# Performance work log

Measured on AMD Instinct MI355X. Metric: run time of the kernel, lower is better.

## Reference

```python
import jax, jax.numpy as jnp
import numpy as np

B, F, K = 8192, 4096, 64


def setup_inputs() -> dict:
    key = jax.random.key(0)
    kx, kv = jax.random.split(key)
    x = jax.random.normal(kx, (B, F), dtype=jnp.float32)
    # original init: uniform(-0.01, 0.01)
    v = jax.random.uniform(kv, (F, K), dtype=jnp.float32, minval=-0.01, maxval=0.01)
    return {"x": x, "v": v}


def reference(x, v):
    # sum_{i<j} <v_i, v_j> x_i x_j  ==  0.5 * sum_f ((x@v)_f^2 - (x^2 @ v^2)_f)
    xv = x @ v                      # [B, K]
    x2v2 = (x * x) @ (v * v)        # [B, K]
    res = 0.5 * jnp.sum(xv * xv - x2v2, axis=-1, keepdims=True)  # [B, 1]
    return res
```

## Files before the change

### kernel.cpp

```cpp
#include <hip/hip_runtime.h>
#include <hip/hip_bf16.h>


#define F_DIM 4096
#define K_DIM 64
#define B_ROWS 8192

typedef __attribute__((ext_vector_type(8))) short short8;
typedef __attribute__((ext_vector_type(4))) float float4v;

__device__ __forceinline__ short f2bs(float f) {
    __hip_bfloat16 h = __float2bfloat16(f);
    short s;
    __builtin_memcpy(&s, &h, 2);
    return s;
}

__global__ void prep_kernel(const float* __restrict__ v,
                            __hip_bfloat16* __restrict__ vt,
                            float* __restrict__ w) {
    const int wave = (blockIdx.x * blockDim.x + threadIdx.x) >> 6;
    const int lane = threadIdx.x & 63;
    if (wave >= F_DIM) return;
    const float val = v[wave * K_DIM + lane];
    float sq = val * val;
#pragma unroll
    for (int m = 32; m >= 1; m >>= 1) sq += __shfl_xor(sq, m, 64);
    if (lane == 0) w[wave] = sq;
    vt[(size_t)lane * F_DIM + wave] = __float2bfloat16(val);
}

__launch_bounds__(512, 4)
__global__ void fm_main_kernel(const float* __restrict__ x,
                               const __hip_bfloat16* __restrict__ vt,
                               const float* __restrict__ w,
                               float* __restrict__ out) {
    __shared__ float yred[8][16][64];
    __shared__ float s2s[16];
    __shared__ float s1s[16];

    const int tid  = threadIdx.x;
    const int lane = tid & 63;
    const int wid  = tid >> 6;
    const int lrow = lane & 15;
    const int lk8  = (lane >> 4) * 8;
    const int row0 = blockIdx.x * 16;

    if (tid < 16) s2s[tid] = 0.0f;
    __syncthreads();

    const float* xrow = x + (size_t)(row0 + lrow) * F_DIM;

    float4v acc0 = {0.f,0.f,0.f,0.f}, acc1 = {0.f,0.f,0.f,0.f};
    float4v acc2 = {0.f,0.f,0.f,0.f}, acc3 = {0.f,0.f,0.f,0.f};
    float s2p = 0.0f;

    const int fbase = wid * (F_DIM / 8);

#pragma unroll 4
    for (int ks = 0; ks < (F_DIM / 8) / 32; ++ks) {
        const int fo = fbase + ks * 32 + lk8;
        const float4v xa = *(const float4v*)(xrow + fo);
        const float4v xb = *(const float4v*)(xrow + fo + 4);
        const float4v wa = *(const float4v*)(w + fo);
        const float4v wb = *(const float4v*)(w + fo + 4);

        s2p += xa.x*xa.x*wa.x + xa.y*xa.y*wa.y + xa.z*xa.z*wa.z + xa.w*xa.w*wa.w
             + xb.x*xb.x*wb.x + xb.y*xb.y*wb.y + xb.z*xb.z*wb.z + xb.w*xb.w*wb.w;

        short8 af;
        af[0]=f2bs(xa.x); af[1]=f2bs(xa.y); af[2]=f2bs(xa.z); af[3]=f2bs(xa.w);
        af[4]=f2bs(xb.x); af[5]=f2bs(xb.y); af[6]=f2bs(xb.z); af[7]=f2bs(xb.w);

        const __hip_bfloat16* bbase = vt + (size_t)lrow * F_DIM + fo;
        const short8 b0 = *(const short8*)(bbase);
        const short8 b1 = *(const short8*)(bbase + 16 * F_DIM);
        const short8 b2 = *(const short8*)(bbase + 32 * F_DIM);
        const short8 b3 = *(const short8*)(bbase + 48 * F_DIM);

        acc0 = __builtin_amdgcn_mfma_f32_16x16x32_bf16(af, b0, acc0, 0, 0, 0);
        acc1 = __builtin_amdgcn_mfma_f32_16x16x32_bf16(af, b1, acc1, 0, 0, 0);
        acc2 = __builtin_amdgcn_mfma_f32_16x16x32_bf16(af, b2, acc2, 0, 0, 0);
        acc3 = __builtin_amdgcn_mfma_f32_16x16x32_bf16(af, b3, acc3, 0, 0, 0);
    }

    s2p += __shfl_xor(s2p, 16, 64);
    s2p += __shfl_xor(s2p, 32, 64);
    if (lane < 16) atomicAdd(&s2s[lrow], s2p);

    const int arow = (lane >> 4) * 4;
#pragma unroll
    for (int r = 0; r < 4; ++r) {
        yred[wid][arow + r][ 0 + lrow] = acc0[r];
        yred[wid][arow + r][16 + lrow] = acc1[r];
        yred[wid][arow + r][32 + lrow] = acc2[r];
        yred[wid][arow + r][48 + lrow] = acc3[r];
    }
    __syncthreads();

#pragma unroll
    for (int half = 0; half < 2; ++half) {
        const int row = wid + half * 8;
        float y = 0.0f;
#pragma unroll
        for (int wv = 0; wv < 8; ++wv) y += yred[wv][row][lane];
        float yy = y * y;
#pragma unroll
        for (int m = 32; m >= 1; m >>= 1) yy += __shfl_xor(yy, m, 64);
        if (lane == 0) s1s[row] = yy;
    }
    __syncthreads();

    if (tid < 16) out[row0 + tid] = 0.5f * (s1s[tid] - s2s[tid]);
}

extern "C" void kernel_launch(void* const* d_in, const int* in_sizes, int n_in,
                              void* d_out, int out_size, void* d_ws, size_t ws_size,
                              hipStream_t stream) {
    const float* x = (const float*)d_in[0];
    const float* v = (const float*)d_in[1];
    float* out = (float*)d_out;

    __hip_bfloat16* vt = (__hip_bfloat16*)d_ws;
    float* w = (float*)((char*)d_ws + (size_t)K_DIM * F_DIM * 2);

    prep_kernel<<<F_DIM / 4, 256, 0, stream>>>(v, vt, w);

    fm_main_kernel<<<B_ROWS / 16, 512, 0, stream>>>(x, vt, w, out);
}
```

Baseline: 209.2 us.

## Switch to 32x32x16 MFMA with 32-row tiles and 16-wave blocks

```diff
diff --git a/kernel.cpp b/kernel.cpp
--- a/kernel.cpp
+++ b/kernel.cpp
@@ -8,6 +8,7 @@
 
 typedef __attribute__((ext_vector_type(8))) short short8;
 typedef __attribute__((ext_vector_type(4))) float float4v;
+typedef __attribute__((ext_vector_type(16))) float f32x16;
 
 __device__ __forceinline__ short f2bs(float f) {
     __hip_bfloat16 h = __float2bfloat16(f);
@@ -30,36 +31,35 @@
     vt[(size_t)lane * F_DIM + wave] = __float2bfloat16(val);
 }
 
-__launch_bounds__(512, 4)
+__launch_bounds__(1024, 4)
 __global__ void fm_main_kernel(const float* __restrict__ x,
                                const __hip_bfloat16* __restrict__ vt,
                                const float* __restrict__ w,
                                float* __restrict__ out) {
-    __shared__ float yred[8][16][64];
-    __shared__ float s2s[16];
-    __shared__ float s1s[16];
+    __shared__ float yred[8][32][64];
+    __shared__ float s1s[32];
+    __shared__ float s2s[32];
 
     const int tid  = threadIdx.x;
     const int lane = tid & 63;
     const int wid  = tid >> 6;
-    const int lrow = lane & 15;
-    const int lk8  = (lane >> 4) * 8;
-    const int row0 = blockIdx.x * 16;
+    const int lrow = lane & 31;
+    const int lk8  = (lane >> 5) * 8;
+    const int row0 = blockIdx.x * 32;
 
-    if (tid < 16) s2s[tid] = 0.0f;
+    if (tid < 32) s2s[tid] = 0.0f;
     __syncthreads();
 
     const float* xrow = x + (size_t)(row0 + lrow) * F_DIM;
+    const int fbase = wid * (F_DIM / 16);
 
-    float4v acc0 = {0.f,0.f,0.f,0.f}, acc1 = {0.f,0.f,0.f,0.f};
-    float4v acc2 = {0.f,0.f,0.f,0.f}, acc3 = {0.f,0.f,0.f,0.f};
+    f32x16 acc0{};
+    f32x16 acc1{};
     float s2p = 0.0f;
 
-    const int fbase = wid * (F_DIM / 8);
-
-#pragma unroll 4
-    for (int ks = 0; ks < (F_DIM / 8) / 32; ++ks) {
-        const int fo = fbase + ks * 32 + lk8;
+#pragma unroll 2
+    for (int ks = 0; ks < 16; ++ks) {
+        const int fo = fbase + ks * 16 + lk8;
         const float4v xa = *(const float4v*)(xrow + fo);
         const float4v xb = *(const float4v*)(xrow + fo + 4);
         const float4v wa = *(const float4v*)(w + fo);
@@ -72,38 +72,43 @@
         af[0]=f2bs(xa.x); af[1]=f2bs(xa.y); af[2]=f2bs(xa.z); af[3]=f2bs(xa.w);
         af[4]=f2bs(xb.x); af[5]=f2bs(xb.y); af[6]=f2bs(xb.z); af[7]=f2bs(xb.w);
 
-        const __hip_bfloat16* bbase = vt + (size_t)lrow * F_DIM + fo;
-        const short8 b0 = *(const short8*)(bbase);
-        const short8 b1 = *(const short8*)(bbase + 16 * F_DIM);
-        const short8 b2 = *(const short8*)(bbase + 32 * F_DIM);
-        const short8 b3 = *(const short8*)(bbase + 48 * F_DIM);
+        const __hip_bfloat16* bb = vt + fo;
+        const short8 b0 = *(const short8*)(bb + (size_t)lrow * F_DIM);
+        const short8 b1 = *(const short8*)(bb + (size_t)(32 + lrow) * F_DIM);
 
-        acc0 = __builtin_amdgcn_mfma_f32_16x16x32_bf16(af, b0, acc0, 0, 0, 0);
-        acc1 = __builtin_amdgcn_mfma_f32_16x16x32_bf16(af, b1, acc1, 0, 0, 0);
-        acc2 = __builtin_amdgcn_mfma_f32_16x16x32_bf16(af, b2, acc2, 0, 0, 0);
-        acc3 = __builtin_amdgcn_mfma_f32_16x16x32_bf16(af, b3, acc3, 0, 0, 0);
+        acc0 = __builtin_amdgcn_mfma_f32_32x32x16_bf16(af, b0, acc0, 0, 0, 0);
+        acc1 = __builtin_amdgcn_mfma_f32_32x32x16_bf16(af, b1, acc1, 0, 0, 0);
     }
 
-    s2p += __shfl_xor(s2p, 16, 64);
     s2p += __shfl_xor(s2p, 32, 64);
-    if (lane < 16) atomicAdd(&s2s[lrow], s2p);
+    if (lane < 32) atomicAdd(&s2s[lrow], s2p);
 
-    const int arow = (lane >> 4) * 4;
+    const int rbase = 4 * (lane >> 5);
+    if (wid < 8) {
 #pragma unroll
-    for (int r = 0; r < 4; ++r) {
-        yred[wid][arow + r][ 0 + lrow] = acc0[r];
-        yred[wid][arow + r][16 + lrow] = acc1[r];
-        yred[wid][arow + r][32 + lrow] = acc2[r];
-        yred[wid][arow + r][48 + lrow] = acc3[r];
+        for (int r = 0; r < 16; ++r) {
+            const int row = (r & 3) + 8 * (r >> 2) + rbase;
+            yred[wid][row][lrow]      = acc0[r];
+            yred[wid][row][32 + lrow] = acc1[r];
+        }
+    }
+    __syncthreads();
+    if (wid >= 8) {
+#pragma unroll
+        for (int r = 0; r < 16; ++r) {
+            const int row = (r & 3) + 8 * (r >> 2) + rbase;
+            yred[wid - 8][row][lrow]      += acc0[r];
+            yred[wid - 8][row][32 + lrow] += acc1[r];
+        }
     }
     __syncthreads();
 
 #pragma unroll
-    for (int half = 0; half < 2; ++half) {
-        const int row = wid + half * 8;
+    for (int h = 0; h < 2; ++h) {
+        const int row = 2 * wid + h;
         float y = 0.0f;
 #pragma unroll
-        for (int wv = 0; wv < 8; ++wv) y += yred[wv][row][lane];
+        for (int s = 0; s < 8; ++s) y += yred[s][row][lane];
         float yy = y * y;
 #pragma unroll
         for (int m = 32; m >= 1; m >>= 1) yy += __shfl_xor(yy, m, 64);
@@ -111,7 +116,7 @@
     }
     __syncthreads();
 
-    if (tid < 16) out[row0 + tid] = 0.5f * (s1s[tid] - s2s[tid]);
+    if (tid < 32) out[row0 + tid] = 0.5f * (s1s[tid] - s2s[tid]);
 }
 
 extern "C" void kernel_launch(void* const* d_in, const int* in_sizes, int n_in,
@@ -125,6 +130,5 @@
     float* w = (float*)((char*)d_ws + (size_t)K_DIM * F_DIM * 2);
 
     prep_kernel<<<F_DIM / 4, 256, 0, stream>>>(v, vt, w);
-
-    fm_main_kernel<<<B_ROWS / 16, 512, 0, stream>>>(x, vt, w, out);
+    fm_main_kernel<<<B_ROWS / 32, 1024, 0, stream>>>(x, vt, w, out);
 }
```

Result: no change. 213.1 us (+1.9%).
